# Performance work log

Hardware: AMD Instinct MI355X
Metric: run time of the kernel (lower is better)

The kernel has to match this reference:

```python
import jax, jax.numpy as jnp
import numpy as np


def setup_inputs() -> dict:
    key = jax.random.key(0)
    ks = jax.random.split(key, 8)
    B = 32768
    return {
        "x": jax.random.normal(ks[0], (B, 784), dtype=jnp.float32),
        "conv_w": jax.random.normal(ks[1], (3, 3), dtype=jnp.float32),
        "fc1_w": jax.random.normal(ks[2], (512, 676), dtype=jnp.float32) * 0.04,
        "fc1_b": jax.random.normal(ks[3], (512,), dtype=jnp.float32),
        "fc2_w": jax.random.normal(ks[4], (512, 512), dtype=jnp.float32) * 0.04,
        "fc2_b": jax.random.normal(ks[5], (512,), dtype=jnp.float32),
        "out_w": jax.random.normal(ks[6], (10, 512), dtype=jnp.float32) * 0.04,
        "out_b": jax.random.normal(ks[7], (10,), dtype=jnp.float32),
    }


def reference(x, conv_w, fc1_w, fc1_b, fc2_w, fc2_b, out_w, out_b):
    B = x.shape[0]
    img = x.reshape(B, 1, 28, 28)  # NCHW, single channel
    # Valid 3x3 cross-correlation (same math as the nested tensordot loop).
    kern = conv_w.reshape(1, 1, 3, 3)  # OIHW
    conv = jax.lax.conv_general_dilated(
        img, kern, window_strides=(1, 1), padding="VALID",
        dimension_numbers=("NCHW", "OIHW", "NCHW"))  # [B,1,26,26]
    h = conv.reshape(B, 26 * 26)
    h = jax.nn.relu(h @ fc1_w.T + fc1_b)
    h = jax.nn.relu(h @ fc2_w.T + fc2_b)
    return h @ out_w.T + out_b  # [B,10] logits
```

## Files before the change

### kernel.cpp

```cpp
#include <hip/hip_runtime.h>

typedef unsigned short ushort_t;
typedef __attribute__((ext_vector_type(8))) short bf16x8;
typedef __attribute__((ext_vector_type(4))) float f32x4;
typedef __attribute__((ext_vector_type(16))) float f32x16;

__device__ __forceinline__ unsigned short f2bf(float f) {
    union { float f; unsigned u; } v; v.f = f;
    unsigned r = v.u + 0x7FFFu + ((v.u >> 16) & 1u);
    return (unsigned short)(r >> 16);
}

__device__ __forceinline__ void gl_lds16(const void* g, void* l) {
    __builtin_amdgcn_global_load_lds(
        (const __attribute__((address_space(1))) unsigned int*)g,
        (__attribute__((address_space(3))) unsigned int*)l, 16, 0, 0);
}

__global__ __launch_bounds__(256) void prep_all(const float* __restrict__ fc1_w,
                                                const float* __restrict__ cw,
                                                const float* __restrict__ fc2_w,
                                                const float* __restrict__ out_w,
                                                ushort_t* __restrict__ W1,
                                                ushort_t* __restrict__ W2,
                                                ushort_t* __restrict__ W3) {
    int idx = blockIdx.x * 256 + threadIdx.x;
    if (idx < 512 * 832) {
        int n = idx / 832, p = idx % 832;
        float acc = 0.f;
        if (p < 784) {
            int pr = p / 28, pc = p % 28;
#pragma unroll
            for (int dr = 0; dr < 3; ++dr) {
                int r = pr - dr;
                if (r < 0 || r >= 26) continue;
#pragma unroll
                for (int dc = 0; dc < 3; ++dc) {
                    int col = pc - dc;
                    if (col < 0 || col >= 26) continue;
                    acc += cw[dr * 3 + dc] * fc1_w[n * 676 + r * 26 + col];
                }
            }
        }
        W1[idx] = f2bf(acc);
    }
    if (idx < 512 * 512) W2[idx] = f2bf(fc2_w[idx]);
    if (idx < 16 * 512)  W3[idx] = (idx < 10 * 512) ? f2bf(out_w[idx]) : (ushort_t)0;
}

__global__ __launch_bounds__(256) void cast_x(const float* __restrict__ x, ushort_t* __restrict__ Xb) {
    int idx = blockIdx.x * 256 + threadIdx.x;
    int m = idx / 208, j = idx % 208;
    if (m >= 32768) return;
    uint2 pack;
    if (j < 196) {
        const float4 v = *(const float4*)&x[(size_t)m * 784 + j * 4];
        pack.x = (unsigned)f2bf(v.x) | ((unsigned)f2bf(v.y) << 16);
        pack.y = (unsigned)f2bf(v.z) | ((unsigned)f2bf(v.w) << 16);
    } else {
        pack.x = 0; pack.y = 0;
    }
    *(uint2*)&Xb[(size_t)m * 832 + j * 4] = pack;
}

template <int LDA, int KSTEPS, bool RELU>
__global__ __launch_bounds__(256) void gemm_bias_act(const ushort_t* __restrict__ A,
                                                     const ushort_t* __restrict__ W,
                                                     const float* __restrict__ bias,
                                                     ushort_t* __restrict__ C) {
    __shared__ ushort_t As[128 * 64];
    __shared__ ushort_t Bs[128 * 64];
    const int tid = threadIdx.x;
    const int wave = tid >> 6, lane = tid & 63;
    const int m0 = blockIdx.x * 128, n0 = blockIdx.y * 128;
    const int srow = lane >> 3;
    const int sseg = lane & 7;
    const int gseg = sseg ^ (srow & 7);
    const int wm = wave >> 1, wn = wave & 1;
    const int r32 = lane & 31, half = lane >> 5;
    f32x16 acc[2][2] = {};

    for (int ks = 0; ks < KSTEPS; ++ks) {
        const int k0 = ks * 64;
#pragma unroll
        for (int t = 0; t < 4; ++t) {
            const int r0 = wave * 32 + t * 8;
            const int row = r0 + srow;
            gl_lds16(A + (size_t)(m0 + row) * LDA + k0 + gseg * 8, &As[r0 * 64]);
            gl_lds16(W + (size_t)(n0 + row) * LDA + k0 + gseg * 8, &Bs[r0 * 64]);
        }
        __syncthreads();
#pragma unroll
        for (int ksub = 0; ksub < 4; ++ksub) {
            const int q = ksub * 2 + half;
            bf16x8 af[2], bfr[2];
#pragma unroll
            for (int i = 0; i < 2; ++i) {
                const int mr = wm * 64 + i * 32 + r32;
                af[i] = *(const bf16x8*)&As[mr * 64 + ((q ^ (mr & 7)) * 8)];
                const int nr = wn * 64 + i * 32 + r32;
                bfr[i] = *(const bf16x8*)&Bs[nr * 64 + ((q ^ (nr & 7)) * 8)];
            }
#pragma unroll
            for (int i = 0; i < 2; ++i)
#pragma unroll
                for (int j = 0; j < 2; ++j)
                    acc[i][j] = __builtin_amdgcn_mfma_f32_32x32x16_bf16(af[i], bfr[j], acc[i][j], 0, 0, 0);
        }
        __syncthreads();
    }

#pragma unroll
    for (int j = 0; j < 2; ++j) {
        const int n = n0 + wn * 64 + j * 32 + r32;
        const float bb = bias[n];
#pragma unroll
        for (int i = 0; i < 2; ++i) {
            const int mbase = m0 + wm * 64 + i * 32 + 4 * half;
#pragma unroll
            for (int reg = 0; reg < 16; ++reg) {
                const int row = mbase + (reg & 3) + 8 * (reg >> 2);
                float v = acc[i][j][reg] + bb;
                if (RELU) v = fmaxf(v, 0.0f);
                C[(size_t)row * 512 + n] = f2bf(v);
            }
        }
    }
}

__global__ __launch_bounds__(256) void head_gemm(const ushort_t* __restrict__ h2,
                                                 const ushort_t* __restrict__ W3,
                                                 const float* __restrict__ ob,
                                                 float* __restrict__ out) {
    __shared__ ushort_t Hs[64 * 520];
    const int tid = threadIdx.x;
    const int wave = tid >> 6, lane = tid & 63;
    const int m0 = blockIdx.x * 64;
    for (int r = wave; r < 64; r += 4)
        gl_lds16(h2 + (size_t)(m0 + r) * 512 + lane * 8, &Hs[r * 520]);
    __syncthreads();
    const int quad = lane >> 4, l16 = lane & 15;
    f32x4 acc = {0.f, 0.f, 0.f, 0.f};
#pragma unroll
    for (int ks = 0; ks < 16; ++ks) {
        bf16x8 a = *(const bf16x8*)&Hs[(wave * 16 + l16) * 520 + ks * 32 + quad * 8];
        bf16x8 b = *(const bf16x8*)&W3[l16 * 512 + ks * 32 + quad * 8];
        acc = __builtin_amdgcn_mfma_f32_16x16x32_bf16(a, b, acc, 0, 0, 0);
    }
    if (l16 < 10) {
        const float bb = ob[l16];
#pragma unroll
        for (int r = 0; r < 4; ++r)
            out[(size_t)(m0 + wave * 16 + quad * 4 + r) * 10 + l16] = acc[r] + bb;
    }
}

extern "C" void kernel_launch(void* const* d_in, const int* in_sizes, int n_in,
                              void* d_out, int out_size, void* d_ws, size_t ws_size,
                              hipStream_t stream) {
    const float* x      = (const float*)d_in[0];
    const float* conv_w = (const float*)d_in[1];
    const float* fc1_w  = (const float*)d_in[2];
    const float* fc1_b  = (const float*)d_in[3];
    const float* fc2_w  = (const float*)d_in[4];
    const float* fc2_b  = (const float*)d_in[5];
    const float* out_w  = (const float*)d_in[6];
    const float* out_b  = (const float*)d_in[7];
    float* out = (float*)d_out;

    ushort_t* W1 = (ushort_t*)d_ws;
    ushort_t* W2 = W1 + 512 * 832;
    ushort_t* W3 = W2 + 512 * 512;
    ushort_t* Xb = W3 + 16 * 512;
    ushort_t* h1 = Xb + (size_t)32768 * 832;
    ushort_t* h2 = Xb;

    prep_all<<<dim3((512 * 832 + 255) / 256), 256, 0, stream>>>(fc1_w, conv_w, fc2_w, out_w, W1, W2, W3);

    cast_x<<<dim3((32768 * 208 + 255) / 256), 256, 0, stream>>>(x, Xb);

    gemm_bias_act<832, 13, true><<<dim3(256, 4), 256, 0, stream>>>(Xb, W1, fc1_b, h1);
    gemm_bias_act<512, 8,  true><<<dim3(256, 4), 256, 0, stream>>>(h1, W2, fc2_b, h2);

    head_gemm<<<dim3(512), 256, 0, stream>>>(h2, W3, out_b, out);
}
```

Measured before the change: 249.9 us.

## Fuse head GEMM into fc2 epilogue with atomics; merge prep and cast kernels

The x-to-bf16 cast is merged into the weight-prep kernel, which also initializes the output with the head bias. The fc2 GEMM now writes its ReLU tile to swizzled LDS instead of global memory. From there it does a partial 10-column head GEMM over its 128-wide N slice and atomically adds the result into the output. This removes the h2 global round-trip and two kernel launches, at the cost of four-way float atomics per output element and nondeterministic summation order.

```diff
diff --git a/kernel.cpp b/kernel.cpp
--- a/kernel.cpp
+++ b/kernel.cpp
@@ -17,14 +17,32 @@
         (__attribute__((address_space(3))) unsigned int*)l, 16, 0, 0);
 }
 
-__global__ __launch_bounds__(256) void prep_all(const float* __restrict__ fc1_w,
-                                                const float* __restrict__ cw,
-                                                const float* __restrict__ fc2_w,
-                                                const float* __restrict__ out_w,
-                                                ushort_t* __restrict__ W1,
-                                                ushort_t* __restrict__ W2,
-                                                ushort_t* __restrict__ W3) {
-    int idx = blockIdx.x * 256 + threadIdx.x;
+__global__ __launch_bounds__(256) void prep_cast(const float* __restrict__ x,
+                                                 const float* __restrict__ fc1_w,
+                                                 const float* __restrict__ cw,
+                                                 const float* __restrict__ fc2_w,
+                                                 const float* __restrict__ out_w,
+                                                 const float* __restrict__ out_b,
+                                                 ushort_t* __restrict__ W1,
+                                                 ushort_t* __restrict__ W2,
+                                                 ushort_t* __restrict__ W3,
+                                                 ushort_t* __restrict__ Xb,
+                                                 float* __restrict__ out) {
+    const int idx = blockIdx.x * 256 + threadIdx.x;
+    {
+        int m = idx / 208, j = idx % 208;
+        if (m < 32768) {
+            uint2 pack;
+            if (j < 196) {
+                const float4 v = *(const float4*)&x[(size_t)m * 784 + j * 4];
+                pack.x = (unsigned)f2bf(v.x) | ((unsigned)f2bf(v.y) << 16);
+                pack.y = (unsigned)f2bf(v.z) | ((unsigned)f2bf(v.w) << 16);
+            } else {
+                pack.x = 0; pack.y = 0;
+            }
+            *(uint2*)&Xb[(size_t)m * 832 + j * 4] = pack;
+        }
+    }
     if (idx < 512 * 832) {
         int n = idx / 832, p = idx % 832;
         float acc = 0.f;
@@ -46,21 +64,10 @@
     }
     if (idx < 512 * 512) W2[idx] = f2bf(fc2_w[idx]);
     if (idx < 16 * 512)  W3[idx] = (idx < 10 * 512) ? f2bf(out_w[idx]) : (ushort_t)0;
-}
-
-__global__ __launch_bounds__(256) void cast_x(const float* __restrict__ x, ushort_t* __restrict__ Xb) {
-    int idx = blockIdx.x * 256 + threadIdx.x;
-    int m = idx / 208, j = idx % 208;
-    if (m >= 32768) return;
-    uint2 pack;
-    if (j < 196) {
-        const float4 v = *(const float4*)&x[(size_t)m * 784 + j * 4];
-        pack.x = (unsigned)f2bf(v.x) | ((unsigned)f2bf(v.y) << 16);
-        pack.y = (unsigned)f2bf(v.z) | ((unsigned)f2bf(v.w) << 16);
-    } else {
-        pack.x = 0; pack.y = 0;
-    }
-    *(uint2*)&Xb[(size_t)m * 832 + j * 4] = pack;
+    if (idx >= 512 * 832 && idx < 512 * 832 + 32768 * 10) {
+        int i = idx - 512 * 832;
+        out[i] = out_b[i % 10];
+    }
 }
 
 template <int LDA, int KSTEPS, bool RELU>
@@ -128,30 +135,92 @@
     }
 }
 
-__global__ __launch_bounds__(256) void head_gemm(const ushort_t* __restrict__ h2,
-                                                 const ushort_t* __restrict__ W3,
-                                                 const float* __restrict__ ob,
-                                                 float* __restrict__ out) {
-    __shared__ ushort_t Hs[64 * 520];
+__global__ __launch_bounds__(256) void gemm2_head(const ushort_t* __restrict__ A,
+                                                  const ushort_t* __restrict__ W,
+                                                  const float* __restrict__ bias,
+                                                  const ushort_t* __restrict__ W3,
+                                                  float* __restrict__ out) {
+    __shared__ ushort_t sh[128 * 128];
+    ushort_t* As = sh;
+    ushort_t* Bs = sh + 128 * 64;
     const int tid = threadIdx.x;
     const int wave = tid >> 6, lane = tid & 63;
-    const int m0 = blockIdx.x * 64;
-    for (int r = wave; r < 64; r += 4)
-        gl_lds16(h2 + (size_t)(m0 + r) * 512 + lane * 8, &Hs[r * 520]);
+    const int m0 = blockIdx.x * 128, n0 = blockIdx.y * 128;
+    const int srow = lane >> 3;
+    const int sseg = lane & 7;
+    const int gseg = sseg ^ (srow & 7);
+    const int wm = wave >> 1, wn = wave & 1;
+    const int r32 = lane & 31, half = lane >> 5;
+    f32x16 acc[2][2] = {};
+
+    for (int ks = 0; ks < 8; ++ks) {
+        const int k0 = ks * 64;
+#pragma unroll
+        for (int t = 0; t < 4; ++t) {
+            const int r0 = wave * 32 + t * 8;
+            const int row = r0 + srow;
+            gl_lds16(A + (size_t)(m0 + row) * 512 + k0 + gseg * 8, &As[r0 * 64]);
+            gl_lds16(W + (size_t)(n0 + row) * 512 + k0 + gseg * 8, &Bs[r0 * 64]);
+        }
+        __syncthreads();
+#pragma unroll
+        for (int ksub = 0; ksub < 4; ++ksub) {
+            const int q = ksub * 2 + half;
+            bf16x8 af[2], bfr[2];
+#pragma unroll
+            for (int i = 0; i < 2; ++i) {
+                const int mr = wm * 64 + i * 32 + r32;
+                af[i] = *(const bf16x8*)&As[mr * 64 + ((q ^ (mr & 7)) * 8)];
+                const int nr = wn * 64 + i * 32 + r32;
+                bfr[i] = *(const bf16x8*)&Bs[nr * 64 + ((q ^ (nr & 7)) * 8)];
+            }
+#pragma unroll
+            for (int i = 0; i < 2; ++i)
+#pragma unroll
+                for (int j = 0; j < 2; ++j)
+                    acc[i][j] = __builtin_amdgcn_mfma_f32_32x32x16_bf16(af[i], bfr[j], acc[i][j], 0, 0, 0);
+        }
+        __syncthreads();
+    }
+
+#pragma unroll
+    for (int j = 0; j < 2; ++j) {
+        const int nl = wn * 64 + j * 32 + r32;
+        const float bb = bias[n0 + nl];
+#pragma unroll
+        for (int i = 0; i < 2; ++i) {
+            const int rbase = wm * 64 + i * 32 + 4 * half;
+#pragma unroll
+            for (int reg = 0; reg < 16; ++reg) {
+                const int row = rbase + (reg & 3) + 8 * (reg >> 2);
+                const int seg = (nl >> 3) ^ (row & 7);
+                sh[row * 128 + seg * 8 + (nl & 7)] = f2bf(fmaxf(acc[i][j][reg] + bb, 0.0f));
+            }
+        }
+    }
     __syncthreads();
+
     const int quad = lane >> 4, l16 = lane & 15;
-    f32x4 acc = {0.f, 0.f, 0.f, 0.f};
-#pragma unroll
-    for (int ks = 0; ks < 16; ++ks) {
-        bf16x8 a = *(const bf16x8*)&Hs[(wave * 16 + l16) * 520 + ks * 32 + quad * 8];
-        bf16x8 b = *(const bf16x8*)&W3[l16 * 512 + ks * 32 + quad * 8];
-        acc = __builtin_amdgcn_mfma_f32_16x16x32_bf16(a, b, acc, 0, 0, 0);
+    f32x4 hacc[2] = {};
+#pragma unroll
+    for (int ksub = 0; ksub < 4; ++ksub) {
+        const bf16x8 b = *(const bf16x8*)&W3[l16 * 512 + n0 + ksub * 32 + quad * 8];
+#pragma unroll
+        for (int f = 0; f < 2; ++f) {
+            const int row = wave * 32 + f * 16 + l16;
+            const int seg = (ksub * 4 + quad) ^ (row & 7);
+            const bf16x8 a = *(const bf16x8*)&sh[row * 128 + seg * 8];
+            hacc[f] = __builtin_amdgcn_mfma_f32_16x16x32_bf16(a, b, hacc[f], 0, 0, 0);
+        }
     }
     if (l16 < 10) {
-        const float bb = ob[l16];
-#pragma unroll
-        for (int r = 0; r < 4; ++r)
-            out[(size_t)(m0 + wave * 16 + quad * 4 + r) * 10 + l16] = acc[r] + bb;
+#pragma unroll
+        for (int f = 0; f < 2; ++f) {
+            const int mb = m0 + wave * 32 + f * 16 + quad * 4;
+#pragma unroll
+            for (int r = 0; r < 4; ++r)
+                atomicAdd(&out[(size_t)(mb + r) * 10 + l16], hacc[f][r]);
+        }
     }
 }
 
@@ -173,14 +242,11 @@
     ushort_t* W3 = W2 + 512 * 512;
     ushort_t* Xb = W3 + 16 * 512;
     ushort_t* h1 = Xb + (size_t)32768 * 832;
-    ushort_t* h2 = Xb;
-
-    prep_all<<<dim3((512 * 832 + 255) / 256), 256, 0, stream>>>(fc1_w, conv_w, fc2_w, out_w, W1, W2, W3);
-
-    cast_x<<<dim3((32768 * 208 + 255) / 256), 256, 0, stream>>>(x, Xb);
+
+    prep_cast<<<dim3((32768 * 208 + 255) / 256), 256, 0, stream>>>(
+        x, fc1_w, conv_w, fc2_w, out_w, out_b, W1, W2, W3, Xb, out);
 
     gemm_bias_act<832, 13, true><<<dim3(256, 4), 256, 0, stream>>>(Xb, W1, fc1_b, h1);
-    gemm_bias_act<512, 8,  true><<<dim3(256, 4), 256, 0, stream>>>(h1, W2, fc2_b, h2);
-
-    head_gemm<<<dim3(512), 256, 0, stream>>>(h2, W3, out_b, out);
-}
+
+    gemm2_head<<<dim3(256, 4), 256, 0, stream>>>(h1, W2, fc2_b, W3, out);
+}
```

After: 238.7 us. 1.05x faster.

## Fuse input cast, both hidden GEMMs and head into one megakernel

Applied to the files above, without the earlier changes.

Replaces the separate x-cast, fc1, fc2 and head kernels with a single kernel. Each 512-thread block owns 64 rows, converts x to bf16 on the fly, and keeps the hidden activations in LDS across layers. This removes the global round trips for Xb, h1 and h2 plus several launches. In exchange each block streams all of W1 and W2 per 64 rows, so weight traffic rises a lot. The launch also uses 136KB of LDS with one block per CU and no double buffering, and only 512 blocks.

```diff
diff --git a/kernel.cpp b/kernel.cpp
--- a/kernel.cpp
+++ b/kernel.cpp
@@ -17,14 +17,14 @@
         (__attribute__((address_space(3))) unsigned int*)l, 16, 0, 0);
 }
 
-__global__ __launch_bounds__(256) void prep_all(const float* __restrict__ fc1_w,
-                                                const float* __restrict__ cw,
-                                                const float* __restrict__ fc2_w,
-                                                const float* __restrict__ out_w,
-                                                ushort_t* __restrict__ W1,
-                                                ushort_t* __restrict__ W2,
-                                                ushort_t* __restrict__ W3) {
-    int idx = blockIdx.x * 256 + threadIdx.x;
+__global__ __launch_bounds__(256) void prep_w(const float* __restrict__ fc1_w,
+                                              const float* __restrict__ cw,
+                                              const float* __restrict__ fc2_w,
+                                              const float* __restrict__ out_w,
+                                              ushort_t* __restrict__ W1,
+                                              ushort_t* __restrict__ W2,
+                                              ushort_t* __restrict__ W3) {
+    const int idx = blockIdx.x * 256 + threadIdx.x;
     if (idx < 512 * 832) {
         int n = idx / 832, p = idx % 832;
         float acc = 0.f;
@@ -48,110 +48,160 @@
     if (idx < 16 * 512)  W3[idx] = (idx < 10 * 512) ? f2bf(out_w[idx]) : (ushort_t)0;
 }
 
-__global__ __launch_bounds__(256) void cast_x(const float* __restrict__ x, ushort_t* __restrict__ Xb) {
-    int idx = blockIdx.x * 256 + threadIdx.x;
-    int m = idx / 208, j = idx % 208;
-    if (m >= 32768) return;
-    uint2 pack;
-    if (j < 196) {
-        const float4 v = *(const float4*)&x[(size_t)m * 784 + j * 4];
-        pack.x = (unsigned)f2bf(v.x) | ((unsigned)f2bf(v.y) << 16);
-        pack.y = (unsigned)f2bf(v.z) | ((unsigned)f2bf(v.w) << 16);
-    } else {
-        pack.x = 0; pack.y = 0;
-    }
-    *(uint2*)&Xb[(size_t)m * 832 + j * 4] = pack;
-}
-
-template <int LDA, int KSTEPS, bool RELU>
-__global__ __launch_bounds__(256) void gemm_bias_act(const ushort_t* __restrict__ A,
-                                                     const ushort_t* __restrict__ W,
-                                                     const float* __restrict__ bias,
-                                                     ushort_t* __restrict__ C) {
-    __shared__ ushort_t As[128 * 64];
-    __shared__ ushort_t Bs[128 * 64];
-    const int tid = threadIdx.x;
-    const int wave = tid >> 6, lane = tid & 63;
-    const int m0 = blockIdx.x * 128, n0 = blockIdx.y * 128;
-    const int srow = lane >> 3;
-    const int sseg = lane & 7;
-    const int gseg = sseg ^ (srow & 7);
-    const int wm = wave >> 1, wn = wave & 1;
-    const int r32 = lane & 31, half = lane >> 5;
-    f32x16 acc[2][2] = {};
-
-    for (int ks = 0; ks < KSTEPS; ++ks) {
-        const int k0 = ks * 64;
-#pragma unroll
-        for (int t = 0; t < 4; ++t) {
-            const int r0 = wave * 32 + t * 8;
-            const int row = r0 + srow;
-            gl_lds16(A + (size_t)(m0 + row) * LDA + k0 + gseg * 8, &As[r0 * 64]);
-            gl_lds16(W + (size_t)(n0 + row) * LDA + k0 + gseg * 8, &Bs[r0 * 64]);
-        }
-        __syncthreads();
-#pragma unroll
-        for (int ksub = 0; ksub < 4; ++ksub) {
-            const int q = ksub * 2 + half;
-            bf16x8 af[2], bfr[2];
-#pragma unroll
-            for (int i = 0; i < 2; ++i) {
-                const int mr = wm * 64 + i * 32 + r32;
-                af[i] = *(const bf16x8*)&As[mr * 64 + ((q ^ (mr & 7)) * 8)];
-                const int nr = wn * 64 + i * 32 + r32;
-                bfr[i] = *(const bf16x8*)&Bs[nr * 64 + ((q ^ (nr & 7)) * 8)];
-            }
-#pragma unroll
-            for (int i = 0; i < 2; ++i)
-#pragma unroll
-                for (int j = 0; j < 2; ++j)
-                    acc[i][j] = __builtin_amdgcn_mfma_f32_32x32x16_bf16(af[i], bfr[j], acc[i][j], 0, 0, 0);
-        }
-        __syncthreads();
-    }
-
-#pragma unroll
-    for (int j = 0; j < 2; ++j) {
-        const int n = n0 + wn * 64 + j * 32 + r32;
-        const float bb = bias[n];
-#pragma unroll
-        for (int i = 0; i < 2; ++i) {
-            const int mbase = m0 + wm * 64 + i * 32 + 4 * half;
-#pragma unroll
-            for (int reg = 0; reg < 16; ++reg) {
-                const int row = mbase + (reg & 3) + 8 * (reg >> 2);
-                float v = acc[i][j][reg] + bb;
-                if (RELU) v = fmaxf(v, 0.0f);
-                C[(size_t)row * 512 + n] = f2bf(v);
-            }
-        }
-    }
-}
-
-__global__ __launch_bounds__(256) void head_gemm(const ushort_t* __restrict__ h2,
-                                                 const ushort_t* __restrict__ W3,
-                                                 const float* __restrict__ ob,
-                                                 float* __restrict__ out) {
-    __shared__ ushort_t Hs[64 * 520];
+__global__ __launch_bounds__(512, 1) void mega(const float* __restrict__ x,
+                                               const ushort_t* __restrict__ W1,
+                                               const ushort_t* __restrict__ W2,
+                                               const ushort_t* __restrict__ W3,
+                                               const float* __restrict__ b1,
+                                               const float* __restrict__ b2,
+                                               const float* __restrict__ ob,
+                                               float* __restrict__ out) {
+    extern __shared__ ushort_t smem[];
+    ushort_t* xs = smem;
+    ushort_t* ws = smem + 4096;
+    ushort_t* hs = smem + 4096 + 32768;
+
     const int tid = threadIdx.x;
     const int wave = tid >> 6, lane = tid & 63;
     const int m0 = blockIdx.x * 64;
-    for (int r = wave; r < 64; r += 4)
-        gl_lds16(h2 + (size_t)(m0 + r) * 512 + lane * 8, &Hs[r * 520]);
+    const int srow = lane >> 3, sseg = lane & 7, gseg = sseg ^ (srow & 7);
+    const int r32 = lane & 31, half = lane >> 5;
+    const int xrow = tid >> 3, xoct = tid & 7;
+
+    f32x16 acc[2][2];
+#pragma unroll
+    for (int i = 0; i < 2; ++i)
+#pragma unroll
+        for (int j = 0; j < 2; ++j)
+#pragma unroll
+            for (int e = 0; e < 16; ++e) acc[i][j][e] = 0.f;
+
+    for (int ks = 0; ks < 13; ++ks) {
+        const int k0 = ks * 64;
+#pragma unroll
+        for (int t = 0; t < 8; ++t) {
+            const int rb = wave * 64 + t * 8;
+            gl_lds16(W1 + (size_t)(rb + srow) * 832 + k0 + gseg * 8, &ws[rb * 64]);
+        }
+        {
+            const int gc = k0 + xoct * 8;
+            bf16x8 xv;
+            if (gc < 784) {
+                const float* xp = &x[(size_t)(m0 + xrow) * 784 + gc];
+                const float4 v0 = *(const float4*)xp;
+                const float4 v1 = *(const float4*)(xp + 4);
+                xv[0] = (short)f2bf(v0.x); xv[1] = (short)f2bf(v0.y);
+                xv[2] = (short)f2bf(v0.z); xv[3] = (short)f2bf(v0.w);
+                xv[4] = (short)f2bf(v1.x); xv[5] = (short)f2bf(v1.y);
+                xv[6] = (short)f2bf(v1.z); xv[7] = (short)f2bf(v1.w);
+            } else {
+#pragma unroll
+                for (int e = 0; e < 8; ++e) xv[e] = 0;
+            }
+            *(bf16x8*)&xs[xrow * 64 + ((xoct ^ (xrow & 7)) * 8)] = xv;
+        }
+        __syncthreads();
+#pragma unroll
+        for (int ksub = 0; ksub < 4; ++ksub) {
+            const int q = 2 * ksub + half;
+            bf16x8 af[2], bw[2];
+#pragma unroll
+            for (int i = 0; i < 2; ++i) {
+                af[i] = *(const bf16x8*)&xs[(i * 32 + r32) * 64 + ((q ^ (r32 & 7)) * 8)];
+                bw[i] = *(const bf16x8*)&ws[(wave * 64 + i * 32 + r32) * 64 + ((q ^ (r32 & 7)) * 8)];
+            }
+#pragma unroll
+            for (int i = 0; i < 2; ++i)
+#pragma unroll
+                for (int j = 0; j < 2; ++j)
+                    acc[i][j] = __builtin_amdgcn_mfma_f32_32x32x16_bf16(af[i], bw[j], acc[i][j], 0, 0, 0);
+        }
+        __syncthreads();
+    }
+
+#pragma unroll
+    for (int j = 0; j < 2; ++j) {
+        const int n = wave * 64 + j * 32 + r32;
+        const float bb = b1[n];
+        const int nseg = n >> 3, nrem = n & 7;
+#pragma unroll
+        for (int i = 0; i < 2; ++i) {
+#pragma unroll
+            for (int reg = 0; reg < 16; ++reg) {
+                const int m = i * 32 + 4 * half + (reg & 3) + 8 * (reg >> 2);
+                hs[m * 512 + ((nseg ^ (m & 7)) * 8) + nrem] = f2bf(fmaxf(acc[i][j][reg] + bb, 0.f));
+            }
+        }
+    }
+#pragma unroll
+    for (int i = 0; i < 2; ++i)
+#pragma unroll
+        for (int j = 0; j < 2; ++j)
+#pragma unroll
+            for (int e = 0; e < 16; ++e) acc[i][j][e] = 0.f;
     __syncthreads();
-    const int quad = lane >> 4, l16 = lane & 15;
-    f32x4 acc = {0.f, 0.f, 0.f, 0.f};
-#pragma unroll
-    for (int ks = 0; ks < 16; ++ks) {
-        bf16x8 a = *(const bf16x8*)&Hs[(wave * 16 + l16) * 520 + ks * 32 + quad * 8];
-        bf16x8 b = *(const bf16x8*)&W3[l16 * 512 + ks * 32 + quad * 8];
-        acc = __builtin_amdgcn_mfma_f32_16x16x32_bf16(a, b, acc, 0, 0, 0);
-    }
-    if (l16 < 10) {
-        const float bb = ob[l16];
-#pragma unroll
-        for (int r = 0; r < 4; ++r)
-            out[(size_t)(m0 + wave * 16 + quad * 4 + r) * 10 + l16] = acc[r] + bb;
+
+    for (int ks = 0; ks < 8; ++ks) {
+        const int k0 = ks * 64;
+#pragma unroll
+        for (int t = 0; t < 8; ++t) {
+            const int rb = wave * 64 + t * 8;
+            gl_lds16(W2 + (size_t)(rb + srow) * 512 + k0 + gseg * 8, &ws[rb * 64]);
+        }
+        __syncthreads();
+#pragma unroll
+        for (int ksub = 0; ksub < 4; ++ksub) {
+            const int q = 2 * ksub + half;
+            const int hq = 8 * ks + q;
+            bf16x8 af[2], bw[2];
+#pragma unroll
+            for (int i = 0; i < 2; ++i) {
+                const int m = i * 32 + r32;
+                af[i] = *(const bf16x8*)&hs[m * 512 + ((hq ^ (m & 7)) * 8)];
+                bw[i] = *(const bf16x8*)&ws[(wave * 64 + i * 32 + r32) * 64 + ((q ^ (r32 & 7)) * 8)];
+            }
+#pragma unroll
+            for (int i = 0; i < 2; ++i)
+#pragma unroll
+                for (int j = 0; j < 2; ++j)
+                    acc[i][j] = __builtin_amdgcn_mfma_f32_32x32x16_bf16(af[i], bw[j], acc[i][j], 0, 0, 0);
+        }
+        __syncthreads();
+    }
+
+#pragma unroll
+    for (int j = 0; j < 2; ++j) {
+        const int n = wave * 64 + j * 32 + r32;
+        const float bb = b2[n];
+        const int nseg = n >> 3, nrem = n & 7;
+#pragma unroll
+        for (int i = 0; i < 2; ++i) {
+#pragma unroll
+            for (int reg = 0; reg < 16; ++reg) {
+                const int m = i * 32 + 4 * half + (reg & 3) + 8 * (reg >> 2);
+                hs[m * 512 + ((nseg ^ (m & 7)) * 8) + nrem] = f2bf(fmaxf(acc[i][j][reg] + bb, 0.f));
+            }
+        }
+    }
+    __syncthreads();
+
+    if (wave < 4) {
+        const int quad = lane >> 4, l16 = lane & 15;
+        const int row = wave * 16 + l16;
+        f32x4 hacc = {0.f, 0.f, 0.f, 0.f};
+#pragma unroll
+        for (int ks = 0; ks < 16; ++ks) {
+            const int seg = 4 * ks + quad;
+            const bf16x8 a = *(const bf16x8*)&hs[row * 512 + ((seg ^ (row & 7)) * 8)];
+            const bf16x8 b = *(const bf16x8*)&W3[l16 * 512 + ks * 32 + quad * 8];
+            hacc = __builtin_amdgcn_mfma_f32_16x16x32_bf16(a, b, hacc, 0, 0, 0);
+        }
+        if (l16 < 10) {
+            const float bb = ob[l16];
+#pragma unroll
+            for (int r = 0; r < 4; ++r)
+                out[(size_t)(m0 + wave * 16 + quad * 4 + r) * 10 + l16] = hacc[r] + bb;
+        }
     }
 }
 
@@ -171,16 +221,8 @@
     ushort_t* W1 = (ushort_t*)d_ws;
     ushort_t* W2 = W1 + 512 * 832;
     ushort_t* W3 = W2 + 512 * 512;
-    ushort_t* Xb = W3 + 16 * 512;
-    ushort_t* h1 = Xb + (size_t)32768 * 832;
-    ushort_t* h2 = Xb;
-
-    prep_all<<<dim3((512 * 832 + 255) / 256), 256, 0, stream>>>(fc1_w, conv_w, fc2_w, out_w, W1, W2, W3);
-
-    cast_x<<<dim3((32768 * 208 + 255) / 256), 256, 0, stream>>>(x, Xb);
-
-    gemm_bias_act<832, 13, true><<<dim3(256, 4), 256, 0, stream>>>(Xb, W1, fc1_b, h1);
-    gemm_bias_act<512, 8,  true><<<dim3(256, 4), 256, 0, stream>>>(h1, W2, fc2_b, h2);
-
-    head_gemm<<<dim3(512), 256, 0, stream>>>(h2, W3, out_b, out);
-}
+
+    prep_w<<<dim3(1664), 256, 0, stream>>>(fc1_w, conv_w, fc2_w, out_w, W1, W2, W3);
+
+    mega<<<dim3(512), 512, 139264, stream>>>(x, W1, W2, W3, fc1_b, fc2_b, out_b, out);
+}
```

Result: faster. 230.5 us (-7.8%).
